# Performance work log

Hardware: AMD Instinct MI355X
Metric: run time of the kernel (lower is better)

Reference implementation:

```python
import jax, jax.numpy as jnp
import numpy as np

T, HID = 2048, 1536
H, DK, DV = 12, 128, 128
KEY_DIM, VAL_DIM = H * DK, H * DV
CONV_K, GEN_RED = 4, 8
EPS = 1e-5


def setup_inputs() -> dict:
    key = jax.random.key(0)
    ks = jax.random.split(key, 12)
    def rn(k, sh, scale):
        return jax.random.normal(k, sh, dtype=jnp.float32) * scale
    inv = HID ** -0.5
    return {
        "hidden_states": rn(ks[0], (T, HID), 1.0),
        "Wq": rn(ks[1], (HID, KEY_DIM), inv),
        "Wk": rn(ks[2], (HID, KEY_DIM), inv),
        "Wv": rn(ks[3], (HID, VAL_DIM), inv),
        "Wb": rn(ks[4], (HID, H), inv),
        "Wa": rn(ks[5], (HID, H), inv),
        "A_log": jnp.log(jax.random.uniform(ks[6], (H,), minval=1e-3, maxval=16.0)),
        "dt_bias": jnp.ones((H,), jnp.float32),
        "Wg1": rn(ks[7], (HID, HID // GEN_RED), inv),
        "Wg2": rn(ks[8], (HID // GEN_RED, VAL_DIM * CONV_K), (HID // GEN_RED) ** -0.5),
        "Wgate": rn(ks[9], (HID, VAL_DIM), inv),
        "norm_weight": jnp.ones((DV,), jnp.float32),
        "Wo": rn(ks[10], (VAL_DIM, HID), VAL_DIM ** -0.5),
    }


def _dynamic_conv(v, hs, Wg1, Wg2):
    # per-token per-channel causal depthwise conv; kernels generated from hidden_states
    w = jax.nn.silu(hs @ Wg1) @ Wg2                    # (T, VAL_DIM*K)
    w = w.reshape(T, VAL_DIM, CONV_K)                  # (T, D, K)
    vpad = jnp.pad(v, ((CONV_K - 1, 0), (0, 0)))       # causal left pad
    windows = jnp.stack([vpad[i:i + T] for i in range(CONV_K)], axis=1)  # (T, K, D)
    return jax.nn.silu(jnp.einsum('tkd,tdk->td', windows, w))


def _gated_delta_rule(q, k, v, g, beta):
    # q,k: (T,H,DK); v: (T,H,DV); g,beta: (T,H)
    scale = DK ** -0.5
    def step(S, inp):
        q_t, k_t, v_t, g_t, b_t = inp
        S = S * jnp.exp(g_t)[:, None, None]            # decay state
        kv = jnp.einsum('hk,hkv->hv', k_t, S)          # k^T S
        S = S + jnp.einsum('hk,hv->hkv', k_t, (v_t - kv) * b_t[:, None])
        o_t = jnp.einsum('hk,hkv->hv', q_t, S) * scale
        return S, o_t
    S0 = jnp.zeros((H, DK, DV), jnp.float32)
    _, o = jax.lax.scan(step, S0, (q, k, v, g, beta))
    return o                                           # (T, H, DV)


def reference(hidden_states, Wq, Wk, Wv, Wb, Wa, A_log, dt_bias,
              Wg1, Wg2, Wgate, norm_weight, Wo):
    hs = hidden_states
    q = jax.nn.silu(hs @ Wq).reshape(T, H, DK)
    k = jax.nn.silu(hs @ Wk).reshape(T, H, DK)
    v = _dynamic_conv(hs @ Wv, hs, Wg1, Wg2).reshape(T, H, DV)
    beta = jax.nn.sigmoid(hs @ Wb)                           # (T, H)
    g = -jnp.exp(A_log) * jax.nn.softplus(hs @ Wa + dt_bias)  # (T, H) log-decay
    o = _gated_delta_rule(q, k, v, g, beta)                  # (T, H, DV)
    # gated RMSNorm over head_v_dim
    gate = (hs @ Wgate).reshape(T, H, DV)
    o = o * jax.lax.rsqrt(jnp.mean(o * o, axis=-1, keepdims=True) + EPS)
    o = o * norm_weight * (gate * jax.nn.sigmoid(gate))
    return o.reshape(T, VAL_DIM) @ Wo
```

## Files before the change

kernel.cpp:

```cpp
#include <hip/hip_runtime.h>
#include <hip/hip_bf16.h>
#include <math.h>

#define T     2048
#define HID   1536
#define NH    12
#define DK    128
#define DV    128
#define CONVK 4
#define CH    64
#define NC    32

typedef __attribute__((ext_vector_type(8))) short bf16x8;
typedef __attribute__((ext_vector_type(8))) _Float16 fp16x8;
typedef __attribute__((ext_vector_type(4))) float floatx4;

__device__ __forceinline__ float siluf(float x) {
    return x / (1.0f + __expf(-x));
}
__device__ __forceinline__ unsigned short f2bf(float f) {
    union { __hip_bfloat16 b; unsigned short u; } cv;
    cv.b = __float2bfloat16(f);
    return cv.u;
}
__device__ __forceinline__ float bf2f(unsigned short u) {
    union { unsigned int u; float f; } cv;
    cv.u = ((unsigned int)u) << 16;
    return cv.f;
}
__device__ __forceinline__ unsigned short f2h(float f) {
    union { _Float16 h; unsigned short u; } cv;
    cv.h = (_Float16)f;
    return cv.u;
}
__device__ __forceinline__ void gl_lds16(const void* g, void* l) {
    __builtin_amdgcn_global_load_lds(
        (const __attribute__((address_space(1))) void*)g,
        (__attribute__((address_space(3))) void*)l, 16, 0, 0);
}
__device__ __forceinline__ void split8_store(const float* xv,
                                             unsigned short* dh, unsigned short* dl) {
    ushort4 h0, h1, l0, l1;
    h0.x = f2bf(xv[0]); l0.x = f2bf(xv[0] - bf2f(h0.x));
    h0.y = f2bf(xv[1]); l0.y = f2bf(xv[1] - bf2f(h0.y));
    h0.z = f2bf(xv[2]); l0.z = f2bf(xv[2] - bf2f(h0.z));
    h0.w = f2bf(xv[3]); l0.w = f2bf(xv[3] - bf2f(h0.w));
    h1.x = f2bf(xv[4]); l1.x = f2bf(xv[4] - bf2f(h1.x));
    h1.y = f2bf(xv[5]); l1.y = f2bf(xv[5] - bf2f(h1.y));
    h1.z = f2bf(xv[6]); l1.z = f2bf(xv[6] - bf2f(h1.z));
    h1.w = f2bf(xv[7]); l1.w = f2bf(xv[7] - bf2f(h1.w));
    *(ushort4*)dh = h0; *(ushort4*)(dh + 4) = h1;
    *(ushort4*)dl = l0; *(ushort4*)(dl + 4) = l1;
}

__global__ __launch_bounds__(256) void splitcast3_kernel(const float* __restrict__ s,
                                                         unsigned short* __restrict__ hi,
                                                         unsigned short* __restrict__ lo,
                                                         unsigned short* __restrict__ h16,
                                                         int n4) {
    int i = blockIdx.x * 256 + threadIdx.x;
    if (i >= n4) return;
    float4 x = ((const float4*)s)[i];
    ushort4 h, l, f;
    h.x = f2bf(x.x); l.x = f2bf(x.x - bf2f(h.x)); f.x = f2h(x.x);
    h.y = f2bf(x.y); l.y = f2bf(x.y - bf2f(h.y)); f.y = f2h(x.y);
    h.z = f2bf(x.z); l.z = f2bf(x.z - bf2f(h.z)); f.z = f2h(x.z);
    h.w = f2bf(x.w); l.w = f2bf(x.w - bf2f(h.w)); f.w = f2h(x.w);
    ((ushort4*)hi)[i] = h;
    ((ushort4*)lo)[i] = l;
    ((ushort4*)h16)[i] = f;
}

__global__ __launch_bounds__(256) void transsplit_kernel(const float* __restrict__ src,
                                                         unsigned short* __restrict__ hi,
                                                         unsigned short* __restrict__ lo,
                                                         int K, int N) {
    __shared__ float tile[32][33];
    const int k0 = blockIdx.y * 32, n0 = blockIdx.x * 32;
    const int tx = threadIdx.x, ty = threadIdx.y;
#pragma unroll
    for (int r = 0; r < 4; ++r) {
        int kk = k0 + ty + 8 * r, nn = n0 + tx;
        tile[ty + 8 * r][tx] = (nn < N) ? src[(size_t)kk * N + nn] : 0.0f;
    }
    __syncthreads();
#pragma unroll
    for (int r = 0; r < 4; ++r) {
        int nn = n0 + ty + 8 * r, kk = k0 + tx;
        if (nn < N) {
            float x = tile[tx][ty + 8 * r];
            unsigned short h = f2bf(x);
            hi[(size_t)nn * K + kk] = h;
            lo[(size_t)nn * K + kk] = f2bf(x - bf2f(h));
        }
    }
}

__global__ __launch_bounds__(256) void transcasth_kernel(const float* __restrict__ src,
                                                         unsigned short* __restrict__ dst,
                                                         int K, int N) {
    __shared__ float tile[32][33];
    const int k0 = blockIdx.y * 32, n0 = blockIdx.x * 32;
    const int tx = threadIdx.x, ty = threadIdx.y;
#pragma unroll
    for (int r = 0; r < 4; ++r) {
        int kk = k0 + ty + 8 * r, nn = n0 + tx;
        tile[ty + 8 * r][tx] = (nn < N) ? src[(size_t)kk * N + nn] : 0.0f;
    }
    __syncthreads();
#pragma unroll
    for (int r = 0; r < 4; ++r) {
        int nn = n0 + ty + 8 * r, kk = k0 + tx;
        if (nn < N) dst[(size_t)nn * K + kk] = f2h(tile[tx][ty + 8 * r]);
    }
}

template<int EPI, int MODE>
__global__ __launch_bounds__(256)
void mgemm(const unsigned short* __restrict__ Ah, const unsigned short* __restrict__ Al,
           const unsigned short* __restrict__ Bh, const unsigned short* __restrict__ Bl,
           int K, int N, float* __restrict__ C, unsigned short* __restrict__ Cb,
           float* __restrict__ qf, float* __restrict__ vf, float* __restrict__ kf,
           unsigned short* __restrict__ gsilb, unsigned short* __restrict__ w1h16,
           float* __restrict__ bgraw)
{
    constexpr int BN   = MODE ? 64 : 128;
    constexpr int BCH  = BN / 16;
    constexpr int NFR  = MODE ? 2 : 4;
    __shared__ unsigned short AsH[2][4096];
    __shared__ unsigned short BsH[2][BCH * 512];
    __shared__ unsigned short AsL[MODE ? 2 : 1][MODE ? 4096 : 4];
    __shared__ unsigned short BsL[MODE ? 2 : 1][MODE ? BCH * 512 : 4];
    const int tid = threadIdx.x;
    const int wave = tid >> 6, lane = tid & 63;
    const int wr = wave >> 1, wc = wave & 1;
    const int lm = lane & 15, lq = lane >> 4;
    const int rowBase = blockIdx.y * 128, colBase = blockIdx.x * BN;

    floatx4 acc[4][NFR];
#pragma unroll
    for (int i = 0; i < 4; ++i)
#pragma unroll
        for (int j = 0; j < NFR; ++j) acc[i][j] = (floatx4){0.f, 0.f, 0.f, 0.f};

    const int mt0 = wave * 2, mt1 = wave * 2 + 1;
    const size_t aOff0 = (size_t)(rowBase + mt0 * 16 + lm) * K + lq * 8;
    const size_t aOff1 = (size_t)(rowBase + mt1 * 16 + lm) * K + lq * 8;
    const size_t bOff0 = (size_t)(colBase + mt0 * 16 + lm) * K + lq * 8;
    const size_t bOff1 = (size_t)(colBase + mt1 * 16 + lm) * K + lq * 8;
    const size_t bOffW = (size_t)(colBase + wave * 16 + lm) * K + lq * 8;

    auto STAGE = [&](int buf, int k0) {
        gl_lds16(Ah + aOff0 + k0, &AsH[buf][mt0 * 512]);
        gl_lds16(Ah + aOff1 + k0, &AsH[buf][mt1 * 512]);
        if (MODE) {
            gl_lds16(Al + aOff0 + k0, &AsL[buf][mt0 * 512]);
            gl_lds16(Al + aOff1 + k0, &AsL[buf][mt1 * 512]);
            gl_lds16(Bh + bOffW + k0, &BsH[buf][wave * 512]);
            gl_lds16(Bl + bOffW + k0, &BsL[buf][wave * 512]);
        } else {
            gl_lds16(Bh + bOff0 + k0, &BsH[buf][mt0 * 512]);
            gl_lds16(Bh + bOff1 + k0, &BsH[buf][mt1 * 512]);
        }
    };

    const int nIter = K >> 5;
    STAGE(0, 0);
    __syncthreads();
    int cur = 0;
    for (int it = 0; it < nIter; ++it) {
        if (it + 1 < nIter) STAGE(cur ^ 1, (it + 1) << 5);
        if (MODE == 0) {
            fp16x8 a[4], b[4];
#pragma unroll
            for (int i = 0; i < 4; ++i) {
                a[i] = *(const fp16x8*)&AsH[cur][(wr * 4 + i) * 512 + lane * 8];
                b[i] = *(const fp16x8*)&BsH[cur][(wc * 4 + i) * 512 + lane * 8];
            }
#pragma unroll
            for (int mi = 0; mi < 4; ++mi)
#pragma unroll
                for (int ni = 0; ni < 4; ++ni)
                    acc[mi][ni] = __builtin_amdgcn_mfma_f32_16x16x32_f16(
                        a[mi], b[ni], acc[mi][ni], 0, 0, 0);
        } else {
            bf16x8 ah[4], al[4], bh[2], bl[2];
#pragma unroll
            for (int i = 0; i < 4; ++i) {
                ah[i] = *(const bf16x8*)&AsH[cur][(wr * 4 + i) * 512 + lane * 8];
                al[i] = *(const bf16x8*)&AsL[cur][(wr * 4 + i) * 512 + lane * 8];
            }
#pragma unroll
            for (int j = 0; j < 2; ++j) {
                bh[j] = *(const bf16x8*)&BsH[cur][(wc * 2 + j) * 512 + lane * 8];
                bl[j] = *(const bf16x8*)&BsL[cur][(wc * 2 + j) * 512 + lane * 8];
            }
#pragma unroll
            for (int mi = 0; mi < 4; ++mi)
#pragma unroll
                for (int ni = 0; ni < 2; ++ni) {
                    acc[mi][ni] = __builtin_amdgcn_mfma_f32_16x16x32_bf16(
                        ah[mi], bh[ni], acc[mi][ni], 0, 0, 0);
                    acc[mi][ni] = __builtin_amdgcn_mfma_f32_16x16x32_bf16(
                        al[mi], bh[ni], acc[mi][ni], 0, 0, 0);
                    acc[mi][ni] = __builtin_amdgcn_mfma_f32_16x16x32_bf16(
                        ah[mi], bl[ni], acc[mi][ni], 0, 0, 0);
                }
        }
        __syncthreads();
        cur ^= 1;
    }

#pragma unroll
    for (int mi = 0; mi < 4; ++mi)
#pragma unroll
        for (int ni = 0; ni < NFR; ++ni) {
            const int col = colBase + wc * (NFR * 16) + ni * 16 + lm;
#pragma unroll
            for (int r = 0; r < 4; ++r) {
                const int row = rowBase + wr * 64 + mi * 16 + lq * 4 + r;
                const float x = acc[mi][ni][r];
                if (EPI == 0) {
                    C[(size_t)row * N + col] = x;
                } else if (EPI == 3) {
                    Cb[(size_t)row * N + col] = f2bf(x);
                } else if (EPI == 1) {
                    if (col < 1536)       qf[(size_t)row * 1536 + col] = siluf(x);
                    else if (col < 3072)  vf[(size_t)row * 1536 + col - 1536] = x;
                    else if (col < 4608)  gsilb[(size_t)row * 1536 + col - 3072] = f2bf(siluf(x));
                    else if (col < 4800)  w1h16[(size_t)row * 192 + col - 4608] = f2h(siluf(x));
                } else {
                    if (col < 1536)       kf[(size_t)row * 1536 + col] = siluf(x);
                    else if (col < 1560)  bgraw[(size_t)row * 24 + col - 1536] = x;
                }
            }
        }
}

__global__ __launch_bounds__(256) void bg2_kernel(const float* __restrict__ bgraw,
                                                  const float* __restrict__ A_log,
                                                  const float* __restrict__ dt_bias,
                                                  float* __restrict__ beta,
                                                  float* __restrict__ g) {
    int idx = blockIdx.x * 256 + threadIdx.x;
    if (idx >= T * 24) return;
    int t = idx / 24, c = idx % 24;
    float x = bgraw[idx];
    if (c < 12) {
        beta[t * NH + c] = 1.0f / (1.0f + __expf(-x));
    } else {
        int h = c - 12;
        float y = x + dt_bias[h];
        float sp = (y > 20.0f) ? y : log1pf(__expf(y));
        g[t * NH + h] = -__expf(A_log[h]) * sp;
    }
}

__global__ __launch_bounds__(256) void conv_kernel(const float* __restrict__ vpre,
                                                   const unsigned short* __restrict__ w,
                                                   float* __restrict__ v) {
    const int idx = blockIdx.x * 256 + threadIdx.x;
    if (idx >= T * HID) return;
    const int t = idx / HID, d = idx % HID;
    const ushort4 wv = *(const ushort4*)(w + (size_t)t * (HID * CONVK) + d * 4);
    const float w4[4] = { bf2f(wv.x), bf2f(wv.y), bf2f(wv.z), bf2f(wv.w) };
    float acc = 0.0f;
#pragma unroll
    for (int i = 0; i < CONVK; i++) {
        const int ts = t - (CONVK - 1) + i;
        if (ts >= 0) acc += vpre[(size_t)ts * HID + d] * w4[i];
    }
    v[idx] = siluf(acc);
}

__global__ __launch_bounds__(256) void prep_kernel(
    const float* __restrict__ q, const float* __restrict__ k,
    unsigned short* __restrict__ Qth, unsigned short* __restrict__ Qtl,
    unsigned short* __restrict__ Kth, unsigned short* __restrict__ Ktl)
{
    __shared__ float KT[128 * 68];
    const int c = blockIdx.x, h = blockIdx.y;
    const int tid = threadIdx.x;
    const size_t tb = (size_t)(h * NC + c) * 8192;

    {
        const int li = tid >> 2, lq4 = tid & 3;
        const float* src = k + (size_t)(c * CH + li) * HID + h * DK + lq4 * 32;
#pragma unroll
        for (int f = 0; f < 8; ++f) {
            float4 x = *(const float4*)(src + f * 4);
            int d0 = lq4 * 32 + f * 4;
            KT[(d0 + 0) * 68 + li] = x.x; KT[(d0 + 1) * 68 + li] = x.y;
            KT[(d0 + 2) * 68 + li] = x.z; KT[(d0 + 3) * 68 + li] = x.w;
        }
    }

#pragma unroll
    for (int e = 0; e < 4; ++e) {
        int u = e * 256 + tid;
        int ch = u >> 6, l = u & 63;
        int i = (ch >> 2) * 16 + (l & 15);
        int dbase = (ch & 3) * 32 + (l >> 4) * 8;
        const float* src = q + (size_t)(c * CH + i) * HID + h * DK + dbase;
        float4 a = *(const float4*)src, b = *(const float4*)(src + 4);
        float xv[8] = {a.x, a.y, a.z, a.w, b.x, b.y, b.z, b.w};
        split8_store(xv, &Qth[tb + ch * 512 + l * 8], &Qtl[tb + ch * 512 + l * 8]);
    }
    __syncthreads();

#pragma unroll
    for (int e = 0; e < 4; ++e) {
        int u = e * 256 + tid;
        int ch = u >> 6, l = u & 63;
        int dk = (ch >> 1) * 16 + (l & 15);
        int ibase = (ch & 1) * 32 + (l >> 4) * 8;
        float4 a = *(const float4*)&KT[dk * 68 + ibase];
        float4 b = *(const float4*)&KT[dk * 68 + ibase + 4];
        float xv[8] = {a.x, a.y, a.z, a.w, b.x, b.y, b.z, b.w};
        split8_store(xv, &Kth[tb + ch * 512 + l * 8], &Ktl[tb + ch * 512 + l * 8]);
    }
}

__global__ __launch_bounds__(256, 1) void chunkloc_kernel(
    const float* __restrict__ q, const float* __restrict__ k, const float* __restrict__ v,
    const float* __restrict__ g, const float* __restrict__ beta,
    float* __restrict__ X1g,
    unsigned short* __restrict__ X2th, unsigned short* __restrict__ X2tl,
    float* __restrict__ Mg, float* __restrict__ csg)
{
    __shared__ unsigned short KhS[64 * 136], KlS[64 * 136];
    __shared__ unsigned short QhS[64 * 136], QlS[64 * 136];
    __shared__ float KT[128 * 68];
    __shared__ float Vs[64 * 132];
    __shared__ float As[64 * 68];
    __shared__ float cs[64], sb[64], sbb[64];

    const int c = blockIdx.x, h = blockIdx.y;
    const int tid = threadIdx.x;
    const int wave = tid >> 6, lane = tid & 63;
    const int lm = lane & 15, lq = lane >> 4;
    const int li = tid >> 2, lq4 = tid & 3;
    const size_t rowbase = (size_t)(c * CH) * HID + h * DK;

    {
        const float* ksrc = k + rowbase + (size_t)li * HID + lq4 * 32;
        const float* qsrc = q + rowbase + (size_t)li * HID + lq4 * 32;
        const float* vsrc = v + (size_t)(c * CH + li) * HID + h * DV + lq4 * 32;
#pragma unroll
        for (int f = 0; f < 8; ++f) {
            float4 kx = *(const float4*)(ksrc + f * 4);
            float4 qx = *(const float4*)(qsrc + f * 4);
            float4 vx = *(const float4*)(vsrc + f * 4);
            const int d0 = lq4 * 32 + f * 4;
            {
                ushort4 hh, ll;
                hh.x = f2bf(kx.x); ll.x = f2bf(kx.x - bf2f(hh.x));
                hh.y = f2bf(kx.y); ll.y = f2bf(kx.y - bf2f(hh.y));
                hh.z = f2bf(kx.z); ll.z = f2bf(kx.z - bf2f(hh.z));
                hh.w = f2bf(kx.w); ll.w = f2bf(kx.w - bf2f(hh.w));
                *(ushort4*)&KhS[li * 136 + d0] = hh;
                *(ushort4*)&KlS[li * 136 + d0] = ll;
            }
            {
                ushort4 hh, ll;
                hh.x = f2bf(qx.x); ll.x = f2bf(qx.x - bf2f(hh.x));
                hh.y = f2bf(qx.y); ll.y = f2bf(qx.y - bf2f(hh.y));
                hh.z = f2bf(qx.z); ll.z = f2bf(qx.z - bf2f(hh.z));
                hh.w = f2bf(qx.w); ll.w = f2bf(qx.w - bf2f(hh.w));
                *(ushort4*)&QhS[li * 136 + d0] = hh;
                *(ushort4*)&QlS[li * 136 + d0] = ll;
            }
            KT[(d0 + 0) * 68 + li] = kx.x;
            KT[(d0 + 1) * 68 + li] = kx.y;
            KT[(d0 + 2) * 68 + li] = kx.z;
            KT[(d0 + 3) * 68 + li] = kx.w;
            *(float4*)&Vs[li * 132 + d0] = vx;
        }
    }
    if (tid < 64) {
        float gv = g[(c * CH + tid) * NH + h];
        float bv = beta[(c * CH + tid) * NH + h];
        float csv = gv;
#pragma unroll
        for (int off = 1; off < 64; off <<= 1) {
            float n = __shfl_up(csv, off);
            if (tid >= off) csv += n;
        }
        cs[tid] = csv; sb[tid] = bv; sbb[tid] = bv * __expf(csv);
    }
    __syncthreads();

    {
        const int ti = wave;
#pragma unroll
        for (int tj = 0; tj < 4; ++tj) {
            floatx4 acc = (floatx4){0.f, 0.f, 0.f, 0.f};
#pragma unroll
            for (int ks = 0; ks < 4; ++ks) {
                bf16x8 a_h = *(const bf16x8*)&KhS[(ti * 16 + lm) * 136 + ks * 32 + lq * 8];
                bf16x8 a_l = *(const bf16x8*)&KlS[(ti * 16 + lm) * 136 + ks * 32 + lq * 8];
                bf16x8 b_h = *(const bf16x8*)&KhS[(tj * 16 + lm) * 136 + ks * 32 + lq * 8];
                bf16x8 b_l = *(const bf16x8*)&KlS[(tj * 16 + lm) * 136 + ks * 32 + lq * 8];
                acc = __builtin_amdgcn_mfma_f32_16x16x32_bf16(a_h, b_h, acc, 0, 0, 0);
                acc = __builtin_amdgcn_mfma_f32_16x16x32_bf16(a_h, b_l, acc, 0, 0, 0);
                acc = __builtin_amdgcn_mfma_f32_16x16x32_bf16(a_l, b_h, acc, 0, 0, 0);
            }
#pragma unroll
            for (int r = 0; r < 4; ++r) {
                const int i = ti * 16 + lq * 4 + r, j = tj * 16 + lm;
                As[i * 68 + j] = (j < i) ? sb[i] * __expf(cs[i] - cs[j]) * acc[r] : 0.0f;
            }
        }
        const size_t mbase = (size_t)(h * NC + c) * CH * CH;
#pragma unroll
        for (int tj = 0; tj < 4; ++tj) {
            floatx4 acc = (floatx4){0.f, 0.f, 0.f, 0.f};
#pragma unroll
            for (int ks = 0; ks < 4; ++ks) {
                bf16x8 a_h = *(const bf16x8*)&QhS[(ti * 16 + lm) * 136 + ks * 32 + lq * 8];
                bf16x8 a_l = *(const bf16x8*)&QlS[(ti * 16 + lm) * 136 + ks * 32 + lq * 8];
                bf16x8 b_h = *(const bf16x8*)&KhS[(tj * 16 + lm) * 136 + ks * 32 + lq * 8];
                bf16x8 b_l = *(const bf16x8*)&KlS[(tj * 16 + lm) * 136 + ks * 32 + lq * 8];
                acc = __builtin_amdgcn_mfma_f32_16x16x32_bf16(a_h, b_h, acc, 0, 0, 0);
                acc = __builtin_amdgcn_mfma_f32_16x16x32_bf16(a_h, b_l, acc, 0, 0, 0);
                acc = __builtin_amdgcn_mfma_f32_16x16x32_bf16(a_l, b_h, acc, 0, 0, 0);
            }
#pragma unroll
            for (int r = 0; r < 4; ++r) {
                const int i = ti * 16 + lq * 4 + r, j = tj * 16 + lm;
                Mg[mbase + (size_t)i * 64 + j] =
                    (j <= i) ? __expf(cs[i] - cs[j]) * acc[r] : 0.0f;
            }
        }
    }

    float xc[64];
    const int col = tid;
    if (col < 128) {
#pragma unroll
        for (int i = 0; i < 64; ++i) xc[i] = sb[i] * Vs[i * 132 + col];
    } else {
        const int dcol = col - 128;
#pragma unroll
        for (int i4 = 0; i4 < 16; ++i4) {
            float4 kq = *(const float4*)&KT[dcol * 68 + i4 * 4];
            xc[i4 * 4 + 0] = sbb[i4 * 4 + 0] * kq.x;
            xc[i4 * 4 + 1] = sbb[i4 * 4 + 1] * kq.y;
            xc[i4 * 4 + 2] = sbb[i4 * 4 + 2] * kq.z;
            xc[i4 * 4 + 3] = sbb[i4 * 4 + 3] * kq.w;
        }
    }
    __syncthreads();

#pragma unroll
    for (int i = 1; i < 64; ++i) {
        float a = xc[i];
#pragma unroll
        for (int j4 = 0; j4 < (i + 3) / 4; ++j4) {
            float4 a4 = *(const float4*)&As[i * 68 + j4 * 4];
            a -= a4.x * xc[j4 * 4 + 0] + a4.y * xc[j4 * 4 + 1]
               + a4.z * xc[j4 * 4 + 2] + a4.w * xc[j4 * 4 + 3];
        }
        xc[i] = a;
    }

    {
        const size_t xbase = (size_t)(h * NC + c) * CH * 128;
        if (col < 128) {
            for (int i = 0; i < 64; ++i) X1g[xbase + (size_t)i * 128 + col] = xc[i];
        } else {
            for (int i = 0; i < 64; ++i) Vs[i * 132 + (col - 128)] = xc[i];
        }
    }
    if (tid < 64) csg[(size_t)(h * NC + c) * CH + tid] = cs[tid];
    __syncthreads();

    {
        const size_t tb = (size_t)(h * NC + c) * 8192;
#pragma unroll
        for (int e = 0; e < 4; ++e) {
            int u = e * 256 + tid;
            int ch = u >> 6, l = u & 63;
            int i = (ch >> 2) * 16 + (l & 15);
            int dbase = (ch & 3) * 32 + (l >> 4) * 8;
            float4 a = *(const float4*)&Vs[i * 132 + dbase];
            float4 b = *(const float4*)&Vs[i * 132 + dbase + 4];
            float xv[8] = {-a.x, -a.y, -a.z, -a.w, -b.x, -b.y, -b.z, -b.w};
            split8_store(xv, &X2th[tb + ch * 512 + l * 8], &X2tl[tb + ch * 512 + l * 8]);
        }
    }
}

__global__ __launch_bounds__(256, 1) void state_kernel(
    const unsigned short* __restrict__ Qth, const unsigned short* __restrict__ Qtl,
    const unsigned short* __restrict__ Kth, const unsigned short* __restrict__ Ktl,
    const unsigned short* __restrict__ X2th, const unsigned short* __restrict__ X2tl,
    float* __restrict__ X1g ,
    const float* __restrict__ csg, float* __restrict__ o)
{
    __shared__ unsigned short SBh[16 * 136], SBl[16 * 136];
    __shared__ unsigned short UBh[16 * 72],  UBl[16 * 72];

    const int h = blockIdx.x, db = blockIdx.y;
    const int tid = threadIdx.x;
    const int wave = tid >> 6, lane = tid & 63;
    const int lm = lane & 15, lq = lane >> 4;

    for (int idx = tid; idx < 16 * 136; idx += 256) { SBh[idx] = 0; SBl[idx] = 0; }
    floatx4 st0 = (floatx4){0.f, 0.f, 0.f, 0.f};
    floatx4 st1 = (floatx4){0.f, 0.f, 0.f, 0.f};
    __syncthreads();

    for (int c = 0; c < NC; ++c) {
        const size_t hc = (size_t)(h * NC + c);
        const size_t xb = hc * CH * 128;
        const size_t tb = hc * 8192 + (size_t)lane * 8;
        const int mw = wave;

        bf16x8 xa_h[4], xa_l[4], qa_h[4], qa_l[4], ka_h[4], ka_l[4];
#pragma unroll
        for (int ks = 0; ks < 4; ++ks) {
            const size_t off = tb + (size_t)(mw * 4 + ks) * 512;
            xa_h[ks] = *(const bf16x8*)(X2th + off);
            xa_l[ks] = *(const bf16x8*)(X2tl + off);
            qa_h[ks] = *(const bf16x8*)(Qth + off);
            qa_l[ks] = *(const bf16x8*)(Qtl + off);
            ka_h[ks] = *(const bf16x8*)(Kth + off);
            ka_l[ks] = *(const bf16x8*)(Ktl + off);
        }
        float x1r[4], csr[4];
#pragma unroll
        for (int r = 0; r < 4; ++r) {
            const int row = mw * 16 + lq * 4 + r;
            x1r[r] = X1g[xb + (size_t)row * 128 + db * 16 + lm];
            csr[r] = csg[hc * CH + row];
        }
        const float cs63 = csg[hc * CH + 63];

        {
            floatx4 accU = (floatx4){0.f, 0.f, 0.f, 0.f};
            floatx4 accO = (floatx4){0.f, 0.f, 0.f, 0.f};
#pragma unroll
            for (int ks = 0; ks < 4; ++ks) {
                bf16x8 sh = *(const bf16x8*)&SBh[lm * 136 + ks * 32 + lq * 8];
                bf16x8 sl = *(const bf16x8*)&SBl[lm * 136 + ks * 32 + lq * 8];
                accU = __builtin_amdgcn_mfma_f32_16x16x32_bf16(xa_h[ks], sh, accU, 0, 0, 0);
                accU = __builtin_amdgcn_mfma_f32_16x16x32_bf16(xa_h[ks], sl, accU, 0, 0, 0);
                accU = __builtin_amdgcn_mfma_f32_16x16x32_bf16(xa_l[ks], sh, accU, 0, 0, 0);
                accO = __builtin_amdgcn_mfma_f32_16x16x32_bf16(qa_h[ks], sh, accO, 0, 0, 0);
                accO = __builtin_amdgcn_mfma_f32_16x16x32_bf16(qa_h[ks], sl, accO, 0, 0, 0);
                accO = __builtin_amdgcn_mfma_f32_16x16x32_bf16(qa_l[ks], sh, accO, 0, 0, 0);
            }
#pragma unroll
            for (int r = 0; r < 4; ++r) {
                const int row = mw * 16 + lq * 4 + r;
                const float u = accU[r] + x1r[r];
                X1g[xb + (size_t)row * 128 + db * 16 + lm] = u;
                const float up = u * __expf(cs63 - csr[r]);
                unsigned short uh = f2bf(up);
                UBh[lm * 72 + row] = uh;
                UBl[lm * 72 + row] = f2bf(up - bf2f(uh));
                o[(size_t)(c * CH + row) * HID + h * DV + db * 16 + lm] =
                    __expf(csr[r]) * accO[r];
            }
        }
        __syncthreads();

        {
            const float bC = __expf(cs63);
#pragma unroll
            for (int mt2 = 0; mt2 < 2; ++mt2) {
                const int mt = wave * 2 + mt2;
                floatx4 acc;
                floatx4 stc = mt2 ? st1 : st0;
#pragma unroll
                for (int r = 0; r < 4; ++r) acc[r] = bC * stc[r];
#pragma unroll
                for (int ks = 0; ks < 2; ++ks) {
                    bf16x8 ah = ka_h[mt2 * 2 + ks];
                    bf16x8 al = ka_l[mt2 * 2 + ks];
                    bf16x8 bh = *(const bf16x8*)&UBh[lm * 72 + ks * 32 + lq * 8];
                    bf16x8 bl = *(const bf16x8*)&UBl[lm * 72 + ks * 32 + lq * 8];
                    acc = __builtin_amdgcn_mfma_f32_16x16x32_bf16(ah, bh, acc, 0, 0, 0);
                    acc = __builtin_amdgcn_mfma_f32_16x16x32_bf16(ah, bl, acc, 0, 0, 0);
                    acc = __builtin_amdgcn_mfma_f32_16x16x32_bf16(al, bh, acc, 0, 0, 0);
                }
                if (mt2) st1 = acc; else st0 = acc;
                ushort4 shv, slv;
#pragma unroll
                for (int r = 0; r < 4; ++r) {
                    const float sv = acc[r];
                    unsigned short sh = f2bf(sv);
                    ((unsigned short*)&shv)[r] = sh;
                    ((unsigned short*)&slv)[r] = f2bf(sv - bf2f(sh));
                }
                const int dkb = mt * 16 + lq * 4;
                *(ushort4*)&SBh[lm * 136 + dkb] = shv;
                *(ushort4*)&SBl[lm * 136 + dkb] = slv;
            }
        }
        __syncthreads();
    }
}

__global__ __launch_bounds__(256) void outk_kernel(
    const float* __restrict__ Ug, const float* __restrict__ Mg,
    float* __restrict__ o)
{
    __shared__ float Msh[64 * 68];
    __shared__ float Ush[64 * 68];

    const int c = blockIdx.x, h = blockIdx.y;
    const int dvb = blockIdx.z * 64;
    const int tid = threadIdx.x;
    const size_t hc = (size_t)(h * NC + c);

    for (int e = 0; e < 16; ++e) {
        int idx = e * 256 + tid;
        Msh[(idx >> 6) * 68 + (idx & 63)] = Mg[hc * CH * CH + idx];
    }
    for (int e = 0; e < 16; ++e) {
        int idx = e * 256 + tid;
        int j = idx >> 6, cc = idx & 63;
        Ush[j * 68 + cc] = Ug[hc * CH * 128 + (size_t)j * 128 + dvb + cc];
    }
    __syncthreads();

    const int tx = tid & 15, ty = tid >> 4;
    const int c0 = tx * 4, i0 = ty * 4;
    float acc[4][4] = {{0}};
    for (int j4 = 0; j4 < 16; ++j4) {
        float uv[4][4];
#pragma unroll
        for (int s = 0; s < 4; ++s) {
            float4 u4 = *(const float4*)&Ush[(j4 * 4 + s) * 68 + c0];
            uv[s][0] = u4.x; uv[s][1] = u4.y; uv[s][2] = u4.z; uv[s][3] = u4.w;
        }
#pragma unroll
        for (int r = 0; r < 4; ++r) {
            float4 m4 = *(const float4*)&Msh[(i0 + r) * 68 + j4 * 4];
            const float mv[4] = {m4.x, m4.y, m4.z, m4.w};
#pragma unroll
            for (int s = 0; s < 4; ++s)
#pragma unroll
                for (int e = 0; e < 4; ++e) acc[r][e] += mv[s] * uv[s][e];
        }
    }
    const float scale = 0.08838834764831845f;
#pragma unroll
    for (int r = 0; r < 4; ++r) {
        float* op = &o[(size_t)(c * CH + i0 + r) * HID + h * DV + dvb + c0];
        float4 prev = *(const float4*)op;
        float4 ov = make_float4(scale * (prev.x + acc[r][0]),
                                scale * (prev.y + acc[r][1]),
                                scale * (prev.z + acc[r][2]),
                                scale * (prev.w + acc[r][3]));
        *(float4*)op = ov;
    }
}

__global__ __launch_bounds__(256) void normgate_kernel(const float* __restrict__ o,
                                                       const unsigned short* __restrict__ gsil,
                                                       const float* __restrict__ nw,
                                                       unsigned short* __restrict__ out_hi,
                                                       unsigned short* __restrict__ out_lo) {
    const int gw = (blockIdx.x * 256 + threadIdx.x) >> 6;
    const int lane = threadIdx.x & 63;
    if (gw >= T * NH) return;
    const int t = gw / NH, h = gw % NH;
    const size_t base = (size_t)t * HID + h * DV;
    const float a = o[base + lane];
    const float b = o[base + lane + 64];
    float ss = a * a + b * b;
    ss += __shfl_xor(ss, 1);  ss += __shfl_xor(ss, 2);  ss += __shfl_xor(ss, 4);
    ss += __shfl_xor(ss, 8);  ss += __shfl_xor(ss, 16); ss += __shfl_xor(ss, 32);
    const float r = rsqrtf(ss * (1.0f / 128.0f) + 1e-5f);
    float va = a * r * nw[lane]      * bf2f(gsil[base + lane]);
    float vb = b * r * nw[lane + 64] * bf2f(gsil[base + lane + 64]);
    unsigned short ha = f2bf(va), hb = f2bf(vb);
    out_hi[base + lane]      = ha;  out_lo[base + lane]      = f2bf(va - bf2f(ha));
    out_hi[base + lane + 64] = hb;  out_lo[base + lane + 64] = f2bf(vb - bf2f(hb));
}

extern "C" void kernel_launch(void* const* d_in, const int* in_sizes, int n_in,
                              void* d_out, int out_size, void* d_ws, size_t ws_size,
                              hipStream_t stream) {
    const float* hs      = (const float*)d_in[0];
    const float* Wq      = (const float*)d_in[1];
    const float* Wk      = (const float*)d_in[2];
    const float* Wv      = (const float*)d_in[3];
    const float* Wb      = (const float*)d_in[4];
    const float* Wa      = (const float*)d_in[5];
    const float* A_log   = (const float*)d_in[6];
    const float* dt_bias = (const float*)d_in[7];
    const float* Wg1     = (const float*)d_in[8];
    const float* Wg2     = (const float*)d_in[9];
    const float* Wgate   = (const float*)d_in[10];
    const float* norm_w  = (const float*)d_in[11];
    const float* Wo      = (const float*)d_in[12];

    float* ws = (float*)d_ws;
    float* q    = ws;
    float* kbuf = ws + 3145728;
    float* vpre = ws + 6291456;
    float* vbuf = ws + 9437184;
    unsigned short* gsil = (unsigned short*)(ws + 12582912);
    float* X1g  = ws + 14155776;
    unsigned short* X2th = (unsigned short*)(ws + 17301504);
    unsigned short* X2tl = (unsigned short*)(ws + 18874368);
    float* Mg   = ws + 20447232;
    unsigned short* WTAfh = (unsigned short*)(ws + 14155776);
    unsigned short* WTBh  = (unsigned short*)(ws + 17891328);
    unsigned short* WTBl  = (unsigned short*)(ws + 19169280);
    unsigned short* wcv   = (unsigned short*)(ws + 14155776);
    unsigned short* WG2h  = (unsigned short*)(ws + 22044672);
    unsigned short* hsh   = (unsigned short*)(ws + 22634496);
    unsigned short* w1h16 = (unsigned short*)(ws + 24207360);
    float* bgraw = ws + 24403968;
    unsigned short* Kth = (unsigned short*)(ws + 22044672);
    unsigned short* Ktl = (unsigned short*)(ws + 23617536);
    float* beta  = ws + 25190400;
    float* g     = ws + 25214976;
    float* csg   = ws + 25239552;
    unsigned short* hsbh = (unsigned short*)(ws + 9437184);
    unsigned short* hsbl = (unsigned short*)(ws + 11010048);
    unsigned short* Qth  = (unsigned short*)(ws + 6291456);
    unsigned short* Qtl  = (unsigned short*)(ws + 7864320);
    unsigned short* WoTh = (unsigned short*)(ws);
    unsigned short* WoTl = (unsigned short*)(ws + 1179648);
    unsigned short* onh  = (unsigned short*)(ws + 6291456);
    unsigned short* onl  = (unsigned short*)(ws + 7864320);

    const dim3 blk(256);
    const dim3 blkT(32, 8);

    splitcast3_kernel<<<3072, blk, 0, stream>>>(hs, hsbh, hsbl, hsh, (T * HID) / 4);
    transcasth_kernel<<<dim3(48, 48), blkT, 0, stream>>>(Wq,    WTAfh,               1536, 1536);
    transcasth_kernel<<<dim3(48, 48), blkT, 0, stream>>>(Wv,    WTAfh + 1536 * 1536, 1536, 1536);
    transcasth_kernel<<<dim3(48, 48), blkT, 0, stream>>>(Wgate, WTAfh + 3072 * 1536, 1536, 1536);
    transcasth_kernel<<<dim3(6, 48),  blkT, 0, stream>>>(Wg1,   WTAfh + 4608 * 1536, 1536, 192);
    transsplit_kernel<<<dim3(48, 48), blkT, 0, stream>>>(Wk, WTBh,               WTBl,               1536, 1536);
    transsplit_kernel<<<dim3(1, 48),  blkT, 0, stream>>>(Wb, WTBh + 1536 * 1536, WTBl + 1536 * 1536, 1536, 12);
    transsplit_kernel<<<dim3(1, 48),  blkT, 0, stream>>>(Wa, WTBh + 1548 * 1536, WTBl + 1548 * 1536, 1536, 12);
    transcasth_kernel<<<dim3(192, 6), blkT, 0, stream>>>(Wg2, WG2h, 192, 6144);

    mgemm<1, 0><<<dim3(38, 16), blk, 0, stream>>>(hsh, nullptr, WTAfh, nullptr, 1536, 4864,
        nullptr, nullptr, q, vpre, nullptr, gsil, w1h16, nullptr);
    mgemm<2, 1><<<dim3(26, 16), blk, 0, stream>>>(hsbh, hsbl, WTBh, WTBl, 1536, 1664,
        nullptr, nullptr, nullptr, nullptr, kbuf, nullptr, nullptr, bgraw);
    bg2_kernel<<<192, blk, 0, stream>>>(bgraw, A_log, dt_bias, beta, g);

    mgemm<3, 0><<<dim3(48, 16), blk, 0, stream>>>(w1h16, nullptr, WG2h, nullptr, 192, 6144,
        nullptr, wcv, nullptr, nullptr, nullptr, nullptr, nullptr, nullptr);
    conv_kernel<<<(T * HID) / 256, blk, 0, stream>>>(vpre, wcv, vbuf);

    chunkloc_kernel<<<dim3(NC, NH), blk, 0, stream>>>(q, kbuf, vbuf, g, beta,
                                                      X1g, X2th, X2tl, Mg, csg);
    prep_kernel<<<dim3(NC, NH), blk, 0, stream>>>(q, kbuf, Qth, Qtl, Kth, Ktl);
    state_kernel<<<dim3(NH, 8), blk, 0, stream>>>(Qth, Qtl, Kth, Ktl, X2th, X2tl,
                                                  X1g, csg, vbuf);
    transsplit_kernel<<<dim3(48, 48), blkT, 0, stream>>>(Wo, WoTh, WoTl, 1536, 1536);
    outk_kernel<<<dim3(NC, NH, 2), blk, 0, stream>>>(X1g, Mg, vbuf);

    normgate_kernel<<<6144, blk, 0, stream>>>(vbuf, gsil, norm_w, onh, onl);
    mgemm<0, 1><<<dim3(24, 16), blk, 0, stream>>>(onh, onl, WoTh, WoTl, 1536, 1536,
        (float*)d_out, nullptr, nullptr, nullptr, nullptr, nullptr, nullptr, nullptr);
}
```

Measured before the change: 585.5 us.

## Double-buffer chunk fragment loads in state kernel to overlap memory with MFMA

Splits the sequential chunk loop of the state kernel into load and compute phases and prefetches the next chunk's Q/K/X2 fragments, X1 values and cumulative decay into a second register set while the current chunk computes. Scheduling barriers keep the compiler from merging the phases. The inner MFMA accumulation is also split into two independent accumulators per output to shorten dependency chains. This doubles fragment register use, which is allowed since the kernel already runs at one block per CU. The prefetched X1 read for chunk c+1 happens before chunk c writes X1, but these touch different chunk rows, so the result is unchanged.

```diff
diff --git a/kernel.cpp b/kernel.cpp
--- a/kernel.cpp
+++ b/kernel.cpp
@@ -491,6 +491,127 @@
     }
 }
 
+struct StFrags {
+    bf16x8 xh[4], xl[4], qh[4], ql[4], kh[4], kl[4];
+    float x1r[4], csr[4], cs63;
+};
+
+__device__ __forceinline__ void st_load(
+    StFrags& f,
+    const unsigned short* __restrict__ Qth, const unsigned short* __restrict__ Qtl,
+    const unsigned short* __restrict__ Kth, const unsigned short* __restrict__ Ktl,
+    const unsigned short* __restrict__ X2th, const unsigned short* __restrict__ X2tl,
+    const float* __restrict__ X1g, const float* __restrict__ csg,
+    int h, int c, int db, int mw, int lane, int lq, int lm)
+{
+    const size_t hc = (size_t)(h * NC + c);
+    const size_t xb = hc * CH * 128;
+    const size_t tb = hc * 8192 + (size_t)lane * 8;
+#pragma unroll
+    for (int ks = 0; ks < 4; ++ks) {
+        const size_t off = tb + (size_t)(mw * 4 + ks) * 512;
+        f.xh[ks] = *(const bf16x8*)(X2th + off);
+        f.xl[ks] = *(const bf16x8*)(X2tl + off);
+        f.qh[ks] = *(const bf16x8*)(Qth + off);
+        f.ql[ks] = *(const bf16x8*)(Qtl + off);
+        f.kh[ks] = *(const bf16x8*)(Kth + off);
+        f.kl[ks] = *(const bf16x8*)(Ktl + off);
+    }
+#pragma unroll
+    for (int r = 0; r < 4; ++r) {
+        const int row = mw * 16 + lq * 4 + r;
+        f.x1r[r] = X1g[xb + (size_t)row * 128 + db * 16 + lm];
+        f.csr[r] = csg[hc * CH + row];
+    }
+    f.cs63 = csg[hc * CH + 63];
+}
+
+__device__ __forceinline__ void st_compute(
+    const StFrags& f, floatx4& st0, floatx4& st1,
+    unsigned short* SBh, unsigned short* SBl,
+    unsigned short* UBh, unsigned short* UBl,
+    float* __restrict__ X1g, float* __restrict__ o,
+    int h, int c, int db, int mw, int lane, int lq, int lm)
+{
+    const size_t hc = (size_t)(h * NC + c);
+    const size_t xb = hc * CH * 128;
+
+    {
+        floatx4 aU0 = (floatx4){0.f, 0.f, 0.f, 0.f};
+        floatx4 aU1 = (floatx4){0.f, 0.f, 0.f, 0.f};
+        floatx4 aO0 = (floatx4){0.f, 0.f, 0.f, 0.f};
+        floatx4 aO1 = (floatx4){0.f, 0.f, 0.f, 0.f};
+#pragma unroll
+        for (int ks = 0; ks < 4; ++ks) {
+            bf16x8 sh = *(const bf16x8*)&SBh[lm * 136 + ks * 32 + lq * 8];
+            bf16x8 sl = *(const bf16x8*)&SBl[lm * 136 + ks * 32 + lq * 8];
+            if (ks & 1) {
+                aU1 = __builtin_amdgcn_mfma_f32_16x16x32_bf16(f.xh[ks], sh, aU1, 0, 0, 0);
+                aU1 = __builtin_amdgcn_mfma_f32_16x16x32_bf16(f.xh[ks], sl, aU1, 0, 0, 0);
+                aU1 = __builtin_amdgcn_mfma_f32_16x16x32_bf16(f.xl[ks], sh, aU1, 0, 0, 0);
+                aO1 = __builtin_amdgcn_mfma_f32_16x16x32_bf16(f.qh[ks], sh, aO1, 0, 0, 0);
+                aO1 = __builtin_amdgcn_mfma_f32_16x16x32_bf16(f.qh[ks], sl, aO1, 0, 0, 0);
+                aO1 = __builtin_amdgcn_mfma_f32_16x16x32_bf16(f.ql[ks], sh, aO1, 0, 0, 0);
+            } else {
+                aU0 = __builtin_amdgcn_mfma_f32_16x16x32_bf16(f.xh[ks], sh, aU0, 0, 0, 0);
+                aU0 = __builtin_amdgcn_mfma_f32_16x16x32_bf16(f.xh[ks], sl, aU0, 0, 0, 0);
+                aU0 = __builtin_amdgcn_mfma_f32_16x16x32_bf16(f.xl[ks], sh, aU0, 0, 0, 0);
+                aO0 = __builtin_amdgcn_mfma_f32_16x16x32_bf16(f.qh[ks], sh, aO0, 0, 0, 0);
+                aO0 = __builtin_amdgcn_mfma_f32_16x16x32_bf16(f.qh[ks], sl, aO0, 0, 0, 0);
+                aO0 = __builtin_amdgcn_mfma_f32_16x16x32_bf16(f.ql[ks], sh, aO0, 0, 0, 0);
+            }
+        }
+#pragma unroll
+        for (int r = 0; r < 4; ++r) {
+            const int row = mw * 16 + lq * 4 + r;
+            const float u = aU0[r] + aU1[r] + f.x1r[r];
+            X1g[xb + (size_t)row * 128 + db * 16 + lm] = u;
+            const float up = u * __expf(f.cs63 - f.csr[r]);
+            unsigned short uh = f2bf(up);
+            UBh[lm * 72 + row] = uh;
+            UBl[lm * 72 + row] = f2bf(up - bf2f(uh));
+            o[(size_t)(c * CH + row) * HID + h * DV + db * 16 + lm] =
+                __expf(f.csr[r]) * (aO0[r] + aO1[r]);
+        }
+    }
+    __syncthreads();
+
+    {
+        const float bC = __expf(f.cs63);
+#pragma unroll
+        for (int mt2 = 0; mt2 < 2; ++mt2) {
+            const int mt = mw * 2 + mt2;
+            floatx4 acc;
+            floatx4 stc = mt2 ? st1 : st0;
+#pragma unroll
+            for (int r = 0; r < 4; ++r) acc[r] = bC * stc[r];
+#pragma unroll
+            for (int ks = 0; ks < 2; ++ks) {
+                bf16x8 ah = f.kh[mt2 * 2 + ks];
+                bf16x8 al = f.kl[mt2 * 2 + ks];
+                bf16x8 bh = *(const bf16x8*)&UBh[lm * 72 + ks * 32 + lq * 8];
+                bf16x8 bl = *(const bf16x8*)&UBl[lm * 72 + ks * 32 + lq * 8];
+                acc = __builtin_amdgcn_mfma_f32_16x16x32_bf16(ah, bh, acc, 0, 0, 0);
+                acc = __builtin_amdgcn_mfma_f32_16x16x32_bf16(ah, bl, acc, 0, 0, 0);
+                acc = __builtin_amdgcn_mfma_f32_16x16x32_bf16(al, bh, acc, 0, 0, 0);
+            }
+            if (mt2) st1 = acc; else st0 = acc;
+            ushort4 shv, slv;
+#pragma unroll
+            for (int r = 0; r < 4; ++r) {
+                const float sv = acc[r];
+                unsigned short sh = f2bf(sv);
+                ((unsigned short*)&shv)[r] = sh;
+                ((unsigned short*)&slv)[r] = f2bf(sv - bf2f(sh));
+            }
+            const int dkb = mt * 16 + lq * 4;
+            *(ushort4*)&SBh[lm * 136 + dkb] = shv;
+            *(ushort4*)&SBl[lm * 136 + dkb] = slv;
+        }
+    }
+    __syncthreads();
+}
+
 __global__ __launch_bounds__(256, 1) void state_kernel(
     const unsigned short* __restrict__ Qth, const unsigned short* __restrict__ Qtl,
     const unsigned short* __restrict__ Kth, const unsigned short* __restrict__ Ktl,
@@ -503,7 +624,7 @@
 
     const int h = blockIdx.x, db = blockIdx.y;
     const int tid = threadIdx.x;
-    const int wave = tid >> 6, lane = tid & 63;
+    const int mw = tid >> 6, lane = tid & 63;
     const int lm = lane & 15, lq = lane >> 4;
 
     for (int idx = tid; idx < 16 * 136; idx += 256) { SBh[idx] = 0; SBl[idx] = 0; }
@@ -511,95 +632,16 @@
     floatx4 st1 = (floatx4){0.f, 0.f, 0.f, 0.f};
     __syncthreads();
 
-    for (int c = 0; c < NC; ++c) {
-        const size_t hc = (size_t)(h * NC + c);
-        const size_t xb = hc * CH * 128;
-        const size_t tb = hc * 8192 + (size_t)lane * 8;
-        const int mw = wave;
-
-        bf16x8 xa_h[4], xa_l[4], qa_h[4], qa_l[4], ka_h[4], ka_l[4];
-#pragma unroll
-        for (int ks = 0; ks < 4; ++ks) {
-            const size_t off = tb + (size_t)(mw * 4 + ks) * 512;
-            xa_h[ks] = *(const bf16x8*)(X2th + off);
-            xa_l[ks] = *(const bf16x8*)(X2tl + off);
-            qa_h[ks] = *(const bf16x8*)(Qth + off);
-            qa_l[ks] = *(const bf16x8*)(Qtl + off);
-            ka_h[ks] = *(const bf16x8*)(Kth + off);
-            ka_l[ks] = *(const bf16x8*)(Ktl + off);
-        }
-        float x1r[4], csr[4];
-#pragma unroll
-        for (int r = 0; r < 4; ++r) {
-            const int row = mw * 16 + lq * 4 + r;
-            x1r[r] = X1g[xb + (size_t)row * 128 + db * 16 + lm];
-            csr[r] = csg[hc * CH + row];
-        }
-        const float cs63 = csg[hc * CH + 63];
-
-        {
-            floatx4 accU = (floatx4){0.f, 0.f, 0.f, 0.f};
-            floatx4 accO = (floatx4){0.f, 0.f, 0.f, 0.f};
-#pragma unroll
-            for (int ks = 0; ks < 4; ++ks) {
-                bf16x8 sh = *(const bf16x8*)&SBh[lm * 136 + ks * 32 + lq * 8];
-                bf16x8 sl = *(const bf16x8*)&SBl[lm * 136 + ks * 32 + lq * 8];
-                accU = __builtin_amdgcn_mfma_f32_16x16x32_bf16(xa_h[ks], sh, accU, 0, 0, 0);
-                accU = __builtin_amdgcn_mfma_f32_16x16x32_bf16(xa_h[ks], sl, accU, 0, 0, 0);
-                accU = __builtin_amdgcn_mfma_f32_16x16x32_bf16(xa_l[ks], sh, accU, 0, 0, 0);
-                accO = __builtin_amdgcn_mfma_f32_16x16x32_bf16(qa_h[ks], sh, accO, 0, 0, 0);
-                accO = __builtin_amdgcn_mfma_f32_16x16x32_bf16(qa_h[ks], sl, accO, 0, 0, 0);
-                accO = __builtin_amdgcn_mfma_f32_16x16x32_bf16(qa_l[ks], sh, accO, 0, 0, 0);
-            }
-#pragma unroll
-            for (int r = 0; r < 4; ++r) {
-                const int row = mw * 16 + lq * 4 + r;
-                const float u = accU[r] + x1r[r];
-                X1g[xb + (size_t)row * 128 + db * 16 + lm] = u;
-                const float up = u * __expf(cs63 - csr[r]);
-                unsigned short uh = f2bf(up);
-                UBh[lm * 72 + row] = uh;
-                UBl[lm * 72 + row] = f2bf(up - bf2f(uh));
-                o[(size_t)(c * CH + row) * HID + h * DV + db * 16 + lm] =
-                    __expf(csr[r]) * accO[r];
-            }
-        }
-        __syncthreads();
-
-        {
-            const float bC = __expf(cs63);
-#pragma unroll
-            for (int mt2 = 0; mt2 < 2; ++mt2) {
-                const int mt = wave * 2 + mt2;
-                floatx4 acc;
-                floatx4 stc = mt2 ? st1 : st0;
-#pragma unroll
-                for (int r = 0; r < 4; ++r) acc[r] = bC * stc[r];
-#pragma unroll
-                for (int ks = 0; ks < 2; ++ks) {
-                    bf16x8 ah = ka_h[mt2 * 2 + ks];
-                    bf16x8 al = ka_l[mt2 * 2 + ks];
-                    bf16x8 bh = *(const bf16x8*)&UBh[lm * 72 + ks * 32 + lq * 8];
-                    bf16x8 bl = *(const bf16x8*)&UBl[lm * 72 + ks * 32 + lq * 8];
-                    acc = __builtin_amdgcn_mfma_f32_16x16x32_bf16(ah, bh, acc, 0, 0, 0);
-                    acc = __builtin_amdgcn_mfma_f32_16x16x32_bf16(ah, bl, acc, 0, 0, 0);
-                    acc = __builtin_amdgcn_mfma_f32_16x16x32_bf16(al, bh, acc, 0, 0, 0);
-                }
-                if (mt2) st1 = acc; else st0 = acc;
-                ushort4 shv, slv;
-#pragma unroll
-                for (int r = 0; r < 4; ++r) {
-                    const float sv = acc[r];
-                    unsigned short sh = f2bf(sv);
-                    ((unsigned short*)&shv)[r] = sh;
-                    ((unsigned short*)&slv)[r] = f2bf(sv - bf2f(sh));
-                }
-                const int dkb = mt * 16 + lq * 4;
-                *(ushort4*)&SBh[lm * 136 + dkb] = shv;
-                *(ushort4*)&SBl[lm * 136 + dkb] = slv;
-            }
-        }
-        __syncthreads();
+    StFrags fA, fB;
+    st_load(fA, Qth, Qtl, Kth, Ktl, X2th, X2tl, X1g, csg, h, 0, db, mw, lane, lq, lm);
+    for (int c = 0; c < NC; c += 2) {
+        st_load(fB, Qth, Qtl, Kth, Ktl, X2th, X2tl, X1g, csg, h, c + 1, db, mw, lane, lq, lm);
+        __builtin_amdgcn_sched_barrier(0);
+        st_compute(fA, st0, st1, SBh, SBl, UBh, UBl, X1g, o, h, c, db, mw, lane, lq, lm);
+        if (c + 2 < NC)
+            st_load(fA, Qth, Qtl, Kth, Ktl, X2th, X2tl, X1g, csg, h, c + 2, db, mw, lane, lq, lm);
+        __builtin_amdgcn_sched_barrier(0);
+        st_compute(fB, st0, st1, SBh, SBl, UBh, UBl, X1g, o, h, c + 1, db, mw, lane, lq, lm);
     }
 }
 
```

New measurement: 544.6 us. -7.0%, faster.
